# Optimization experiments

Measured on AMD Instinct MI355X. Metric: run time of the kernel, lower is better.

## Reference

```python
import jax, jax.numpy as jnp
import numpy as np

B, N, E, ED, H, HID, OUT = 128, 100, 3200, 8, 4, 16, 32


def _ln(x, g, b):
    m = x.mean(-1, keepdims=True)
    v = ((x - m) ** 2).mean(-1, keepdims=True)
    return (x - m) / jnp.sqrt(v + 1e-5) * g + b


def _seg_softmax(logits, seg, n):
    # logits: [Etot, H], seg: [Etot] target node ids
    m = jax.ops.segment_max(logits, seg, num_segments=n)
    ex = jnp.exp(logits - m[seg])
    s = jax.ops.segment_sum(ex, seg, num_segments=n)
    return ex / (s[seg] + 1e-16)


def _tconv(x, src, dst, ea, Wq, bq, Wk, bk, Wv, bv, We, Ws, bs, heads, ch, n):
    # PyG TransformerConv, concat=False, root_weight=True, beta=False
    q = (x @ Wq.T + bq).reshape(-1, heads, ch)
    k = (x @ Wk.T + bk).reshape(-1, heads, ch)
    v = (x @ Wv.T + bv).reshape(-1, heads, ch)
    e = (ea @ We.T).reshape(-1, heads, ch)
    alpha = (q[dst] * (k[src] + e)).sum(-1) / jnp.sqrt(jnp.float32(ch))  # [Etot,H]
    alpha = _seg_softmax(alpha, dst, n)
    msg = (v[src] + e) * alpha[..., None]
    out = jax.ops.segment_sum(msg, dst, num_segments=n)  # [n,H,ch]
    out = out.mean(axis=1)  # concat=False -> head mean
    return out + x @ Ws.T + bs


def setup_inputs() -> dict:
    key = jax.random.key(0)
    ks = jax.random.split(key, 32)
    d = {}
    d['nodes_feats'] = jax.random.randint(ks[0], (B, N, 1), 0, 5).astype(jnp.float32)
    d['edge_index'] = jax.random.randint(ks[1], (B, 2, E), 0, N).astype(jnp.int32)
    d['edge_attr'] = jax.random.normal(ks[2], (B, E, ED), jnp.float32)
    d['agent_id'] = jax.random.randint(ks[3], (B, 1), 0, N).astype(jnp.int32)
    s = 0.1
    d['entity_embed'] = jax.random.normal(ks[4], (5, 4), jnp.float32)
    d['W1'] = jax.random.normal(ks[5], (HID, 4 + ED), jnp.float32) * s
    d['b1'] = jnp.zeros((HID,), jnp.float32)
    d['W2'] = jax.random.normal(ks[6], (HID, HID), jnp.float32) * s
    d['b2'] = jnp.zeros((HID,), jnp.float32)
    d['W3'] = jax.random.normal(ks[7], (HID, HID), jnp.float32) * s
    d['b3'] = jnp.zeros((HID,), jnp.float32)
    d['ln_g'] = jnp.ones((HID,), jnp.float32)
    d['ln_b'] = jnp.zeros((HID,), jnp.float32)
    i = 8
    for pre, ch, outd in (('g1', HID, HID), ('g2', OUT, OUT)):
        d[pre + '_Wq'] = jax.random.normal(ks[i + 0], (H * ch, HID), jnp.float32) * s
        d[pre + '_bq'] = jnp.zeros((H * ch,), jnp.float32)
        d[pre + '_Wk'] = jax.random.normal(ks[i + 1], (H * ch, HID), jnp.float32) * s
        d[pre + '_bk'] = jnp.zeros((H * ch,), jnp.float32)
        d[pre + '_Wv'] = jax.random.normal(ks[i + 2], (H * ch, HID), jnp.float32) * s
        d[pre + '_bv'] = jnp.zeros((H * ch,), jnp.float32)
        d[pre + '_We'] = jax.random.normal(ks[i + 3], (H * ch, ED), jnp.float32) * s
        d[pre + '_Ws'] = jax.random.normal(ks[i + 4], (outd, HID), jnp.float32) * s
        d[pre + '_bs'] = jnp.zeros((outd,), jnp.float32)
        i += 5
    return d


def reference(nodes_feats, edge_index, edge_attr, agent_id, entity_embed,
              W1, b1, W2, b2, W3, b3, ln_g, ln_b,
              g1_Wq, g1_bq, g1_Wk, g1_bk, g1_Wv, g1_bv, g1_We, g1_Ws, g1_bs,
              g2_Wq, g2_bq, g2_Wk, g2_bk, g2_Wv, g2_bv, g2_We, g2_Ws, g2_bs):
    n_tot = B * N
    # batched graph -> flat graph with per-batch node offsets
    offs = (jnp.arange(B, dtype=edge_index.dtype) * N)[:, None, None]
    ei = (edge_index + offs).transpose(1, 0, 2).reshape(2, -1)  # [2, B*E]
    src, dst = ei[0], ei[1]
    x = nodes_feats.reshape(-1, 1)            # [n_tot, 1]
    ea = edge_attr.reshape(-1, ED)            # [B*E, ED]

    # Embedding message-passing layer (aggr='add')
    etype = x[:, 0].astype(jnp.int32)[src]
    emb = entity_embed[etype]                  # [Etot, 4]
    h = jnp.concatenate([emb, ea], axis=1)
    h = _ln(jax.nn.relu(h @ W1.T + b1), ln_g, ln_b)
    h = _ln(jax.nn.relu(h @ W2.T + b2), ln_g, ln_b)
    h = _ln(jax.nn.relu(h @ W3.T + b3), ln_g, ln_b)
    z = jax.ops.segment_sum(h, dst, num_segments=n_tot)  # [n_tot, 16]

    a = _tconv(z, src, dst, ea, g1_Wq, g1_bq, g1_Wk, g1_bk, g1_Wv, g1_bv,
               g1_We, g1_Ws, g1_bs, H, HID, n_tot)
    a = _tconv(a, src, dst, ea, g2_Wq, g2_bq, g2_Wk, g2_bk, g2_Wv, g2_bv,
               g2_We, g2_Ws, g2_bs, H, OUT, n_tot)
    a = jax.nn.relu(a).reshape(B, N, OUT)
    # graph_aggr == 'agent': gather the agent node per batch
    out = jnp.take_along_axis(a, agent_id[:, :, None].astype(jnp.int32), axis=1)
    return out[:, 0, :]  # [B, OUT]
```

## Files before the change

kernel.cpp:

```cpp
#include <hip/hip_runtime.h>
#include <math.h>
#include <stdint.h>

#define Bb   128
#define Nn   100
#define Ee   3200
#define NTOT (Bb*Nn)
#define ETOT (Bb*Ee)



__global__ __launch_bounds__(1024) void k_csr(const int* __restrict__ ei,
                                              const int* __restrict__ agent,
                                              int* __restrict__ off,
                                              int2* __restrict__ cpair,
                                              int* __restrict__ mark)
{
    int b = ((blockIdx.x & 7) << 4) + (blockIdx.x >> 3);
    int t = threadIdx.x;
    __shared__ int s_src[Ee];
    __shared__ int s_dst[Ee];
    __shared__ int cnt[128];
    __shared__ int exc[128];
    __shared__ int cur[128];
    if (t < 128) cnt[t] = 0;
    if (t < Nn) mark[b * Nn + t] = 0;
    __syncthreads();
    const int* eis = ei + (size_t)b * 2 * Ee;
    const int* eid = eis + Ee;
    for (int e = t; e < Ee; e += 1024) {
        int s = eis[e];
        int d = eid[e];
        s_src[e] = s;
        s_dst[e] = d;
        atomicAdd(&cnt[d], 1);
    }
    __syncthreads();
    if (t < 64) {
        int c0 = cnt[2 * t];
        int c1 = cnt[2 * t + 1];
        int p = c0 + c1;
#pragma unroll
        for (int d = 1; d < 64; d <<= 1) {
            int v = __shfl_up(p, d);
            if (t >= d) p += v;
        }
        exc[2 * t]     = p - c0 - c1;
        exc[2 * t + 1] = p - c1;
        cur[2 * t]     = p - c0 - c1;
        cur[2 * t + 1] = p - c1;
    }
    __syncthreads();
    if (t < Nn) off[b * Nn + t] = b * Ee + exc[t];
    if (b == Bb - 1 && t == 0) off[NTOT] = ETOT;
    for (int e = t; e < Ee; e += 1024) {
        int d = s_dst[e];
        int idx = atomicAdd(&cur[d], 1);
        cpair[b * Ee + idx] = make_int2(s_src[e] + b * Nn, b * Ee + e);
    }
    int an = agent[b];
    if (t == 0) mark[b * Nn + an] = 1;
    for (int e = t; e < Ee; e += 1024) {
        if (s_dst[e] == an) mark[b * Nn + s_src[e]] = 1;
    }
}


__device__ __forceinline__ void ln_reg(float* h, const float* __restrict__ g,
                                       const float* __restrict__ b) {
    float s = 0.f;
#pragma unroll
    for (int c = 0; c < 16; c++) s += h[c];
    float m = s * 0.0625f;
    float v = 0.f;
#pragma unroll
    for (int c = 0; c < 16; c++) { float d = h[c] - m; v += d * d; }
    float r = rsqrtf(v * 0.0625f + 1e-5f);
#pragma unroll
    for (int c = 0; c < 16; c++) h[c] = (h[c] - m) * r * g[c] + b[c];
}

__global__ __launch_bounds__(256) void k_mlpz(
    const float* __restrict__ nf, const float* __restrict__ ea, const float* __restrict__ ee,
    const float* __restrict__ W1, const float* __restrict__ b1,
    const float* __restrict__ W2, const float* __restrict__ b2,
    const float* __restrict__ W3, const float* __restrict__ b3,
    const float* __restrict__ lg, const float* __restrict__ lb,
    const float* __restrict__ Wk, const float* __restrict__ bk,
    const float* __restrict__ Wv, const float* __restrict__ bv,
    const int* __restrict__ off, const int2* __restrict__ cpair,
    float* __restrict__ z, float* __restrict__ k1, float* __restrict__ v1)
{
    int lane = threadIdx.x & 63;
    int wid  = threadIdx.x >> 6;
    int n    = (blockIdx.x & 7) * (NTOT / 8) + (blockIdx.x >> 3) * 4 + wid;

    int o0 = off[n];
    int deg = off[n + 1] - o0;
    int chunks = (deg + 63) >> 6;

    float zs[16];
#pragma unroll
    for (int c = 0; c < 16; c++) zs[c] = 0.f;

    for (int ch = 0; ch < chunks; ch++) {
        int i = ch * 64 + lane;
        float h3[16];
        if (i < deg) {
            int2 p = cpair[o0 + i];
            int et = (int)nf[p.x];
            float in[12];
#pragma unroll
            for (int j = 0; j < 4; j++) in[j] = ee[et * 4 + j];
            const float4* ea4 = (const float4*)(ea + (size_t)p.y * 8);
            float4 ua = ea4[0], ub = ea4[1];
            in[4] = ua.x; in[5] = ua.y; in[6] = ua.z; in[7] = ua.w;
            in[8] = ub.x; in[9] = ub.y; in[10] = ub.z; in[11] = ub.w;

            float h1[16];
#pragma unroll
            for (int c = 0; c < 16; c++) {
                float s = b1[c];
#pragma unroll
                for (int j = 0; j < 12; j++) s = fmaf(W1[c * 12 + j], in[j], s);
                h1[c] = fmaxf(s, 0.f);
            }
            ln_reg(h1, lg, lb);
            float h2[16];
#pragma unroll
            for (int c = 0; c < 16; c++) {
                float s = b2[c];
#pragma unroll
                for (int j = 0; j < 16; j++) s = fmaf(W2[c * 16 + j], h1[j], s);
                h2[c] = fmaxf(s, 0.f);
            }
            ln_reg(h2, lg, lb);
#pragma unroll
            for (int c = 0; c < 16; c++) {
                float s = b3[c];
#pragma unroll
                for (int j = 0; j < 16; j++) s = fmaf(W3[c * 16 + j], h2[j], s);
                h3[c] = fmaxf(s, 0.f);
            }
            ln_reg(h3, lg, lb);
        } else {
#pragma unroll
            for (int c = 0; c < 16; c++) h3[c] = 0.f;
        }
#pragma unroll
        for (int c = 0; c < 16; c++) {
            float s = h3[c];
            s += __shfl_xor(s, 1);
            s += __shfl_xor(s, 2);
            s += __shfl_xor(s, 4);
            s += __shfl_xor(s, 8);
            s += __shfl_xor(s, 16);
            s += __shfl_xor(s, 32);
            zs[c] += s;
        }
    }

#pragma unroll
    for (int c = 0; c < 16; c++) if (lane == c) z[n * 16 + c] = zs[c];

    float ak = bk[lane], av = bv[lane];
#pragma unroll
    for (int j = 0; j < 16; j++) {
        ak = fmaf(Wk[lane * 16 + j], zs[j], ak);
        av = fmaf(Wv[lane * 16 + j], zs[j], av);
    }
    k1[n * 64 + lane] = ak;
    v1[n * 64 + lane] = av;
}


__global__ __launch_bounds__(256) void k_attn1(
    const float* __restrict__ ea,
    const float* __restrict__ k1, const float* __restrict__ v1,
    const float* __restrict__ z, const int* __restrict__ mark,
    const float* __restrict__ Wq, const float* __restrict__ bq,
    const float* __restrict__ We, const float* __restrict__ Ws, const float* __restrict__ bs,
    const int* __restrict__ off, const int2* __restrict__ cpair,
    float* __restrict__ a1)
{
    int n = (blockIdx.x & 7) * (NTOT / 8) + (blockIdx.x >> 3);
    if (!mark[n]) return;

    __shared__ float sm[4][64], sl[4][64], sa[4][64];
    int lane = threadIdx.x & 63;
    int w    = threadIdx.x >> 6;

    float zz[16];
#pragma unroll
    for (int j = 0; j < 16; j++) zz[j] = z[n * 16 + j];
    float ql = bq[lane];
#pragma unroll
    for (int j = 0; j < 16; j++) ql = fmaf(Wq[lane * 16 + j], zz[j], ql);
    float wer[8];
#pragma unroll
    for (int j = 0; j < 8; j++) wer[j] = We[lane * 8 + j];

    int o0  = off[n];
    int deg = off[n + 1] - o0;
    int i    = o0 + ((deg * w) >> 2);
    int iend = o0 + ((deg * (w + 1)) >> 2);

    float m = -1e30f, l = 0.f, acc = 0.f;
    for (; i + 2 <= iend; i += 2) {
        int2 pA = cpair[i];
        int2 pB = cpair[i + 1];
        const float4* eaA = (const float4*)(ea + (size_t)pA.y * 8);
        const float4* eaB = (const float4*)(ea + (size_t)pB.y * 8);
        float4 a0v = eaA[0], a1v = eaA[1], b0v = eaB[0], b1v = eaB[1];
        float eA = wer[0] * a0v.x + wer[1] * a0v.y + wer[2] * a0v.z + wer[3] * a0v.w
                 + wer[4] * a1v.x + wer[5] * a1v.y + wer[6] * a1v.z + wer[7] * a1v.w;
        float eB = wer[0] * b0v.x + wer[1] * b0v.y + wer[2] * b0v.z + wer[3] * b0v.w
                 + wer[4] * b1v.x + wer[5] * b1v.y + wer[6] * b1v.z + wer[7] * b1v.w;
        float kA = k1[(size_t)pA.x * 64 + lane];
        float kB = k1[(size_t)pB.x * 64 + lane];
        float vA = v1[(size_t)pA.x * 64 + lane];
        float vB = v1[(size_t)pB.x * 64 + lane];
        float tA = ql * (kA + eA);
        float tB = ql * (kB + eB);
        tA += __shfl_xor(tA, 1, 16);  tB += __shfl_xor(tB, 1, 16);
        tA += __shfl_xor(tA, 2, 16);  tB += __shfl_xor(tB, 2, 16);
        tA += __shfl_xor(tA, 4, 16);  tB += __shfl_xor(tB, 4, 16);
        tA += __shfl_xor(tA, 8, 16);  tB += __shfl_xor(tB, 8, 16);
        float lA  = tA * 0.25f;
        float lBv = tB * 0.25f;
        float nm = fmaxf(m, fmaxf(lA, lBv));
        float sc = __expf(m - nm);
        float wA = __expf(lA - nm);
        float wB = __expf(lBv - nm);
        acc = acc * sc + wA * (vA + eA) + wB * (vB + eB);
        l   = l * sc + wA + wB;
        m   = nm;
    }
    for (; i < iend; i++) {
        int2 p = cpair[i];
        const float4* ea4 = (const float4*)(ea + (size_t)p.y * 8);
        float4 u0 = ea4[0], u1 = ea4[1];
        float el = wer[0] * u0.x + wer[1] * u0.y + wer[2] * u0.z + wer[3] * u0.w
                 + wer[4] * u1.x + wer[5] * u1.y + wer[6] * u1.z + wer[7] * u1.w;
        float kl = k1[(size_t)p.x * 64 + lane];
        float tq = ql * (kl + el);
        tq += __shfl_xor(tq, 1, 16);
        tq += __shfl_xor(tq, 2, 16);
        tq += __shfl_xor(tq, 4, 16);
        tq += __shfl_xor(tq, 8, 16);
        float logit = tq * 0.25f;
        float nm = fmaxf(m, logit);
        float sc = __expf(m - nm);
        float wv = __expf(logit - nm);
        float vl = v1[(size_t)p.x * 64 + lane];
        acc = acc * sc + wv * (vl + el);
        l   = l * sc + wv;
        m   = nm;
    }
    sm[w][lane] = m; sl[w][lane] = l; sa[w][lane] = acc;
    __syncthreads();
    if (w == 0) {
        float M = fmaxf(fmaxf(sm[0][lane], sm[1][lane]), fmaxf(sm[2][lane], sm[3][lane]));
        float L = 0.f, A = 0.f;
#pragma unroll
        for (int ww = 0; ww < 4; ww++) {
            float sc = __expf(sm[ww][lane] - M);
            L += sc * sl[ww][lane];
            A += sc * sa[ww][lane];
        }
        float y = (deg > 0) ? (A / L) : 0.f;
        y += __shfl_xor(y, 16);
        y += __shfl_xor(y, 32);
        y *= 0.25f;
        if (lane < 16) {
            float r = bs[lane];
#pragma unroll
            for (int j = 0; j < 16; j++) r = fmaf(Ws[lane * 16 + j], zz[j], r);
            a1[n * 16 + lane] = y + r;
        }
    }
}


__global__ __launch_bounds__(512) void k_g2(
    const float* __restrict__ ea, const float* __restrict__ a1, const int* __restrict__ agent,
    const float* __restrict__ Wq, const float* __restrict__ bq,
    const float* __restrict__ Wk, const float* __restrict__ bk,
    const float* __restrict__ Wv, const float* __restrict__ bv,
    const float* __restrict__ We, const float* __restrict__ Ws, const float* __restrict__ bs,
    const int* __restrict__ off, const int2* __restrict__ cpair,
    float* __restrict__ out)
{
    __shared__ float sm[8][64], sl[8][64], sa0[8][64], sa1[8][64];
    int b = ((blockIdx.x & 7) << 4) + (blockIdx.x >> 3);
    int lane = threadIdx.x & 63;
    int w = threadIdx.x >> 6;
    int n = b * Nn + agent[b];
    int v0 = lane * 2, v1i = lane * 2 + 1;

    float aa[16];
#pragma unroll
    for (int j = 0; j < 16; j++) aa[j] = a1[n * 16 + j];

    float wk0[16], wk1[16], wv0[16], wv1[16], we0[8], we1[8];
#pragma unroll
    for (int j = 0; j < 16; j++) {
        wk0[j] = Wk[v0 * 16 + j];  wk1[j] = Wk[v1i * 16 + j];
        wv0[j] = Wv[v0 * 16 + j];  wv1[j] = Wv[v1i * 16 + j];
    }
#pragma unroll
    for (int j = 0; j < 8; j++) { we0[j] = We[v0 * 8 + j]; we1[j] = We[v1i * 8 + j]; }

    float q0 = bq[v0], q1v = bq[v1i];
#pragma unroll
    for (int j = 0; j < 16; j++) {
        q0  = fmaf(Wq[v0 * 16 + j],  aa[j], q0);
        q1v = fmaf(Wq[v1i * 16 + j], aa[j], q1v);
    }

    int o0 = off[n];
    int deg = off[n + 1] - o0;

    float m = -1e30f, l = 0.f, a0 = 0.f, a1c = 0.f;
    for (int i = w; i < deg; i += 8) {
        int2 p = cpair[o0 + i];
        int src = p.x, ge = p.y;
        float as[16];
#pragma unroll
        for (int j = 0; j < 16; j++) as[j] = a1[src * 16 + j];
        const float4* ea4 = (const float4*)(ea + (size_t)ge * 8);
        float4 u0 = ea4[0], u1 = ea4[1];
        float eav[8] = {u0.x, u0.y, u0.z, u0.w, u1.x, u1.y, u1.z, u1.w};

        float k0 = bk[v0], k1v = bk[v1i], vv0 = bv[v0], vv1 = bv[v1i];
#pragma unroll
        for (int j = 0; j < 16; j++) {
            k0  = fmaf(wk0[j], as[j], k0);
            k1v = fmaf(wk1[j], as[j], k1v);
            vv0 = fmaf(wv0[j], as[j], vv0);
            vv1 = fmaf(wv1[j], as[j], vv1);
        }
        float e0 = 0.f, e1 = 0.f;
#pragma unroll
        for (int j = 0; j < 8; j++) { e0 = fmaf(we0[j], eav[j], e0); e1 = fmaf(we1[j], eav[j], e1); }

        float t = q0 * (k0 + e0) + q1v * (k1v + e1);
        t += __shfl_xor(t, 1, 16);
        t += __shfl_xor(t, 2, 16);
        t += __shfl_xor(t, 4, 16);
        t += __shfl_xor(t, 8, 16);
        float logit = t * 0.17677669529663687f;
        float nm = fmaxf(m, logit);
        float sc = __expf(m - nm);
        float wgt = __expf(logit - nm);
        a0  = a0 * sc + wgt * (vv0 + e0);
        a1c = a1c * sc + wgt * (vv1 + e1);
        l   = l * sc + wgt;
        m   = nm;
    }
    sm[w][lane] = m; sl[w][lane] = l; sa0[w][lane] = a0; sa1[w][lane] = a1c;
    __syncthreads();
    if (w == 0) {
        float M = sm[0][lane];
#pragma unroll
        for (int ww = 1; ww < 8; ww++) M = fmaxf(M, sm[ww][lane]);
        float L = 0.f, A0 = 0.f, A1 = 0.f;
#pragma unroll
        for (int ww = 0; ww < 8; ww++) {
            float sc = __expf(sm[ww][lane] - M);
            L  += sc * sl[ww][lane];
            A0 += sc * sa0[ww][lane];
            A1 += sc * sa1[ww][lane];
        }
        float y0 = (deg > 0) ? (A0 / L) : 0.f;
        float y1 = (deg > 0) ? (A1 / L) : 0.f;
        y0 += __shfl_xor(y0, 16); y0 += __shfl_xor(y0, 32);
        y1 += __shfl_xor(y1, 16); y1 += __shfl_xor(y1, 32);
        y0 *= 0.25f; y1 *= 0.25f;

        if (lane < 16) {
            int c0 = lane * 2, c1 = lane * 2 + 1;
            float r0 = bs[c0], r1 = bs[c1];
#pragma unroll
            for (int j = 0; j < 16; j++) {
                r0 = fmaf(Ws[c0 * 16 + j], aa[j], r0);
                r1 = fmaf(Ws[c1 * 16 + j], aa[j], r1);
            }
            out[b * 32 + c0] = fmaxf(y0 + r0, 0.f);
            out[b * 32 + c1] = fmaxf(y1 + r1, 0.f);
        }
    }
}


extern "C" void kernel_launch(void* const* d_in, const int* in_sizes, int n_in,
                              void* d_out, int out_size, void* d_ws, size_t ws_size,
                              hipStream_t stream) {
    (void)in_sizes; (void)n_in; (void)out_size; (void)ws_size;
    const float* nf    = (const float*)d_in[0];
    const int*   ei    = (const int*)d_in[1];
    const float* ea    = (const float*)d_in[2];
    const int*   agent = (const int*)d_in[3];
    const float* ee    = (const float*)d_in[4];
    const float* W1    = (const float*)d_in[5];
    const float* b1    = (const float*)d_in[6];
    const float* W2    = (const float*)d_in[7];
    const float* b2    = (const float*)d_in[8];
    const float* W3    = (const float*)d_in[9];
    const float* b3    = (const float*)d_in[10];
    const float* lg    = (const float*)d_in[11];
    const float* lb    = (const float*)d_in[12];
    const float* g1Wq  = (const float*)d_in[13];
    const float* g1bq  = (const float*)d_in[14];
    const float* g1Wk  = (const float*)d_in[15];
    const float* g1bk  = (const float*)d_in[16];
    const float* g1Wv  = (const float*)d_in[17];
    const float* g1bv  = (const float*)d_in[18];
    const float* g1We  = (const float*)d_in[19];
    const float* g1Ws  = (const float*)d_in[20];
    const float* g1bs  = (const float*)d_in[21];
    const float* g2Wq  = (const float*)d_in[22];
    const float* g2bq  = (const float*)d_in[23];
    const float* g2Wk  = (const float*)d_in[24];
    const float* g2bk  = (const float*)d_in[25];
    const float* g2Wv  = (const float*)d_in[26];
    const float* g2bv  = (const float*)d_in[27];
    const float* g2We  = (const float*)d_in[28];
    const float* g2Ws  = (const float*)d_in[29];
    const float* g2bs  = (const float*)d_in[30];
    float* out = (float*)d_out;

    char* w = (char*)d_ws;
    int* mark  = (int*)w;  w += (size_t)NTOT * 4;
    int* off   = (int*)w;  w += (size_t)(NTOT + 4) * 4;
    w = (char*)(((uintptr_t)w + 15) & ~(uintptr_t)15);
    int2* cpair = (int2*)w; w += (size_t)ETOT * 8;
    float* z   = (float*)w; w += (size_t)NTOT * 16 * 4;
    float* k1  = (float*)w; w += (size_t)NTOT * 64 * 4;
    float* v1  = (float*)w; w += (size_t)NTOT * 64 * 4;
    float* a1  = (float*)w; w += (size_t)NTOT * 16 * 4;

    k_csr<<<dim3(Bb), dim3(1024), 0, stream>>>(ei, agent, off, cpair, mark);
    k_mlpz<<<dim3(NTOT / 4), dim3(256), 0, stream>>>(
        nf, ea, ee, W1, b1, W2, b2, W3, b3, lg, lb,
        g1Wk, g1bk, g1Wv, g1bv,
        off, cpair, z, k1, v1);
    k_attn1<<<dim3(NTOT), dim3(256), 0, stream>>>(
        ea, k1, v1, z, mark,
        g1Wq, g1bq, g1We, g1Ws, g1bs,
        off, cpair, a1);
    k_g2<<<dim3(Bb), dim3(512), 0, stream>>>(
        ea, a1, agent, g2Wq, g2bq, g2Wk, g2bk, g2Wv, g2bv, g2We, g2Ws, g2bs,
        off, cpair, out);
}
```

Before: 193.7 us.

## Fuse CSR build with edge MLP and compact marked-node list for attention

Merges the CSR construction kernel and the per-node edge-MLP/z aggregation into one kernel per graph. That kernel computes the edge MLP in original edge order, reduces z with shared-memory atomics, and computes k1/v1 from shared z. It also builds a compact list of nodes that need layer-1 attention, so attn1 launches 128*50 blocks that loop over listed nodes instead of NTOT blocks that mostly exit early. This removes one launch and the CSR gather indirection in the MLP. In exchange, 128 blocks of 512 threads may underfill the GPU for the MLP work, and shared atomics can contend.

```diff
diff --git a/kernel.cpp b/kernel.cpp
--- a/kernel.cpp
+++ b/kernel.cpp
@@ -9,63 +9,6 @@
 #define ETOT (Bb*Ee)
 
 
-
-__global__ __launch_bounds__(1024) void k_csr(const int* __restrict__ ei,
-                                              const int* __restrict__ agent,
-                                              int* __restrict__ off,
-                                              int2* __restrict__ cpair,
-                                              int* __restrict__ mark)
-{
-    int b = ((blockIdx.x & 7) << 4) + (blockIdx.x >> 3);
-    int t = threadIdx.x;
-    __shared__ int s_src[Ee];
-    __shared__ int s_dst[Ee];
-    __shared__ int cnt[128];
-    __shared__ int exc[128];
-    __shared__ int cur[128];
-    if (t < 128) cnt[t] = 0;
-    if (t < Nn) mark[b * Nn + t] = 0;
-    __syncthreads();
-    const int* eis = ei + (size_t)b * 2 * Ee;
-    const int* eid = eis + Ee;
-    for (int e = t; e < Ee; e += 1024) {
-        int s = eis[e];
-        int d = eid[e];
-        s_src[e] = s;
-        s_dst[e] = d;
-        atomicAdd(&cnt[d], 1);
-    }
-    __syncthreads();
-    if (t < 64) {
-        int c0 = cnt[2 * t];
-        int c1 = cnt[2 * t + 1];
-        int p = c0 + c1;
-#pragma unroll
-        for (int d = 1; d < 64; d <<= 1) {
-            int v = __shfl_up(p, d);
-            if (t >= d) p += v;
-        }
-        exc[2 * t]     = p - c0 - c1;
-        exc[2 * t + 1] = p - c1;
-        cur[2 * t]     = p - c0 - c1;
-        cur[2 * t + 1] = p - c1;
-    }
-    __syncthreads();
-    if (t < Nn) off[b * Nn + t] = b * Ee + exc[t];
-    if (b == Bb - 1 && t == 0) off[NTOT] = ETOT;
-    for (int e = t; e < Ee; e += 1024) {
-        int d = s_dst[e];
-        int idx = atomicAdd(&cur[d], 1);
-        cpair[b * Ee + idx] = make_int2(s_src[e] + b * Nn, b * Ee + e);
-    }
-    int an = agent[b];
-    if (t == 0) mark[b * Nn + an] = 1;
-    for (int e = t; e < Ee; e += 1024) {
-        if (s_dst[e] == an) mark[b * Nn + s_src[e]] = 1;
-    }
-}
-
-
 __device__ __forceinline__ void ln_reg(float* h, const float* __restrict__ g,
                                        const float* __restrict__ b) {
     float s = 0.f;
@@ -80,7 +23,9 @@
     for (int c = 0; c < 16; c++) h[c] = (h[c] - m) * r * g[c] + b[c];
 }
 
-__global__ __launch_bounds__(256) void k_mlpz(
+
+__global__ __launch_bounds__(512) void k_cmz(
+    const int* __restrict__ ei, const int* __restrict__ agent,
     const float* __restrict__ nf, const float* __restrict__ ea, const float* __restrict__ ee,
     const float* __restrict__ W1, const float* __restrict__ b1,
     const float* __restrict__ W2, const float* __restrict__ b2,
@@ -88,196 +33,256 @@
     const float* __restrict__ lg, const float* __restrict__ lb,
     const float* __restrict__ Wk, const float* __restrict__ bk,
     const float* __restrict__ Wv, const float* __restrict__ bv,
-    const int* __restrict__ off, const int2* __restrict__ cpair,
+    int* __restrict__ off, int2* __restrict__ cpair,
+    int* __restrict__ mlist, int* __restrict__ mcnt,
     float* __restrict__ z, float* __restrict__ k1, float* __restrict__ v1)
 {
-    int lane = threadIdx.x & 63;
-    int wid  = threadIdx.x >> 6;
-    int n    = (blockIdx.x & 7) * (NTOT / 8) + (blockIdx.x >> 3) * 4 + wid;
-
-    int o0 = off[n];
-    int deg = off[n + 1] - o0;
-    int chunks = (deg + 63) >> 6;
-
-    float zs[16];
-#pragma unroll
-    for (int c = 0; c < 16; c++) zs[c] = 0.f;
-
-    for (int ch = 0; ch < chunks; ch++) {
-        int i = ch * 64 + lane;
+    int b = ((blockIdx.x & 7) << 4) + (blockIdx.x >> 3);
+    int t = threadIdx.x;
+    __shared__ int   s_src[Ee];
+    __shared__ int   s_dst[Ee];
+    __shared__ float zl[Nn][17];
+    __shared__ int   cnt[128], exc[128], cur[128];
+    __shared__ int   smark[Nn], slist[Nn];
+    __shared__ int   scnt;
+
+    for (int i = t; i < Nn * 17; i += 512) ((float*)zl)[i] = 0.f;
+    if (t < 128) cnt[t] = 0;
+    if (t < Nn)  smark[t] = 0;
+    if (t == 0)  scnt = 0;
+    __syncthreads();
+
+    const int* eis = ei + (size_t)b * 2 * Ee;
+    const int* eid = eis + Ee;
+    for (int e = t; e < Ee; e += 512) {
+        int s = eis[e];
+        int d = eid[e];
+        s_src[e] = s;
+        s_dst[e] = d;
+        atomicAdd(&cnt[d], 1);
+    }
+    __syncthreads();
+    if (t < 64) {
+        int c0 = cnt[2 * t];
+        int c1 = cnt[2 * t + 1];
+        int p = c0 + c1;
+#pragma unroll
+        for (int d = 1; d < 64; d <<= 1) {
+            int v = __shfl_up(p, d);
+            if (t >= d) p += v;
+        }
+        exc[2 * t]     = p - c0 - c1;
+        exc[2 * t + 1] = p - c1;
+        cur[2 * t]     = p - c0 - c1;
+        cur[2 * t + 1] = p - c1;
+    }
+    __syncthreads();
+    if (t < Nn) off[b * Nn + t] = b * Ee + exc[t];
+    if (b == Bb - 1 && t == 0) off[NTOT] = ETOT;
+    for (int e = t; e < Ee; e += 512) {
+        int d = s_dst[e];
+        int idx = atomicAdd(&cur[d], 1);
+        cpair[b * Ee + idx] = make_int2(s_src[e] + b * Nn, b * Ee + e);
+    }
+    int an = agent[b];
+    if (t == 0) {
+        int old = atomicExch(&smark[an], 1);
+        if (!old) { int ix = atomicAdd(&scnt, 1); slist[ix] = an; }
+    }
+    for (int e = t; e < Ee; e += 512) {
+        if (s_dst[e] == an) {
+            int s = s_src[e];
+            int old = atomicExch(&smark[s], 1);
+            if (!old) { int ix = atomicAdd(&scnt, 1); slist[ix] = s; }
+        }
+    }
+    for (int e = t; e < Ee; e += 512) {
+        int src = s_src[e];
+        int dst = s_dst[e];
+        int et = (int)nf[b * Nn + src];
+        float in[12];
+#pragma unroll
+        for (int j = 0; j < 4; j++) in[j] = ee[et * 4 + j];
+        const float4* ea4 = (const float4*)(ea + ((size_t)b * Ee + e) * 8);
+        float4 ua = ea4[0], ub = ea4[1];
+        in[4] = ua.x; in[5] = ua.y; in[6] = ua.z; in[7] = ua.w;
+        in[8] = ub.x; in[9] = ub.y; in[10] = ub.z; in[11] = ub.w;
+
+        float h1[16];
+#pragma unroll
+        for (int c = 0; c < 16; c++) {
+            float s = b1[c];
+#pragma unroll
+            for (int j = 0; j < 12; j++) s = fmaf(W1[c * 12 + j], in[j], s);
+            h1[c] = fmaxf(s, 0.f);
+        }
+        ln_reg(h1, lg, lb);
+        float h2[16];
+#pragma unroll
+        for (int c = 0; c < 16; c++) {
+            float s = b2[c];
+#pragma unroll
+            for (int j = 0; j < 16; j++) s = fmaf(W2[c * 16 + j], h1[j], s);
+            h2[c] = fmaxf(s, 0.f);
+        }
+        ln_reg(h2, lg, lb);
         float h3[16];
-        if (i < deg) {
-            int2 p = cpair[o0 + i];
-            int et = (int)nf[p.x];
-            float in[12];
-#pragma unroll
-            for (int j = 0; j < 4; j++) in[j] = ee[et * 4 + j];
-            const float4* ea4 = (const float4*)(ea + (size_t)p.y * 8);
-            float4 ua = ea4[0], ub = ea4[1];
-            in[4] = ua.x; in[5] = ua.y; in[6] = ua.z; in[7] = ua.w;
-            in[8] = ub.x; in[9] = ub.y; in[10] = ub.z; in[11] = ub.w;
-
-            float h1[16];
-#pragma unroll
-            for (int c = 0; c < 16; c++) {
-                float s = b1[c];
-#pragma unroll
-                for (int j = 0; j < 12; j++) s = fmaf(W1[c * 12 + j], in[j], s);
-                h1[c] = fmaxf(s, 0.f);
+#pragma unroll
+        for (int c = 0; c < 16; c++) {
+            float s = b3[c];
+#pragma unroll
+            for (int j = 0; j < 16; j++) s = fmaf(W3[c * 16 + j], h2[j], s);
+            h3[c] = fmaxf(s, 0.f);
+        }
+        ln_reg(h3, lg, lb);
+#pragma unroll
+        for (int c = 0; c < 16; c++) atomicAdd(&zl[dst][c], h3[c]);
+    }
+    __syncthreads();
+
+    if (t < scnt) mlist[b * Nn + t] = slist[t];
+    if (t == 0)   mcnt[b] = scnt;
+
+    {
+        int ch = t & 63;
+        int n0 = t >> 6;
+        float wkr[16], wvr[16];
+#pragma unroll
+        for (int j = 0; j < 16; j++) { wkr[j] = Wk[ch * 16 + j]; wvr[j] = Wv[ch * 16 + j]; }
+        float bkv = bk[ch], bvv = bv[ch];
+        for (int n = n0; n < Nn; n += 8) {
+            float zz[16];
+#pragma unroll
+            for (int j = 0; j < 16; j++) zz[j] = zl[n][j];
+            if (ch < 16) z[((size_t)b * Nn + n) * 16 + ch] = zl[n][ch];
+            float ak = bkv, av = bvv;
+#pragma unroll
+            for (int j = 0; j < 16; j++) {
+                ak = fmaf(wkr[j], zz[j], ak);
+                av = fmaf(wvr[j], zz[j], av);
             }
-            ln_reg(h1, lg, lb);
-            float h2[16];
-#pragma unroll
-            for (int c = 0; c < 16; c++) {
-                float s = b2[c];
-#pragma unroll
-                for (int j = 0; j < 16; j++) s = fmaf(W2[c * 16 + j], h1[j], s);
-                h2[c] = fmaxf(s, 0.f);
-            }
-            ln_reg(h2, lg, lb);
-#pragma unroll
-            for (int c = 0; c < 16; c++) {
-                float s = b3[c];
-#pragma unroll
-                for (int j = 0; j < 16; j++) s = fmaf(W3[c * 16 + j], h2[j], s);
-                h3[c] = fmaxf(s, 0.f);
-            }
-            ln_reg(h3, lg, lb);
-        } else {
-#pragma unroll
-            for (int c = 0; c < 16; c++) h3[c] = 0.f;
-        }
-#pragma unroll
-        for (int c = 0; c < 16; c++) {
-            float s = h3[c];
-            s += __shfl_xor(s, 1);
-            s += __shfl_xor(s, 2);
-            s += __shfl_xor(s, 4);
-            s += __shfl_xor(s, 8);
-            s += __shfl_xor(s, 16);
-            s += __shfl_xor(s, 32);
-            zs[c] += s;
-        }
-    }
-
-#pragma unroll
-    for (int c = 0; c < 16; c++) if (lane == c) z[n * 16 + c] = zs[c];
-
-    float ak = bk[lane], av = bv[lane];
-#pragma unroll
-    for (int j = 0; j < 16; j++) {
-        ak = fmaf(Wk[lane * 16 + j], zs[j], ak);
-        av = fmaf(Wv[lane * 16 + j], zs[j], av);
-    }
-    k1[n * 64 + lane] = ak;
-    v1[n * 64 + lane] = av;
+            k1[((size_t)b * Nn + n) * 64 + ch] = ak;
+            v1[((size_t)b * Nn + n) * 64 + ch] = av;
+        }
+    }
 }
 
 
 __global__ __launch_bounds__(256) void k_attn1(
     const float* __restrict__ ea,
     const float* __restrict__ k1, const float* __restrict__ v1,
-    const float* __restrict__ z, const int* __restrict__ mark,
+    const float* __restrict__ z,
+    const int* __restrict__ mlist, const int* __restrict__ mcnt,
     const float* __restrict__ Wq, const float* __restrict__ bq,
     const float* __restrict__ We, const float* __restrict__ Ws, const float* __restrict__ bs,
     const int* __restrict__ off, const int2* __restrict__ cpair,
     float* __restrict__ a1)
 {
-    int n = (blockIdx.x & 7) * (NTOT / 8) + (blockIdx.x >> 3);
-    if (!mark[n]) return;
-
     __shared__ float sm[4][64], sl[4][64], sa[4][64];
+    int bl   = blockIdx.x & 127;
+    int rep  = blockIdx.x >> 7;
+    int b    = ((bl & 7) << 4) + (bl >> 3);
     int lane = threadIdx.x & 63;
     int w    = threadIdx.x >> 6;
-
-    float zz[16];
-#pragma unroll
-    for (int j = 0; j < 16; j++) zz[j] = z[n * 16 + j];
-    float ql = bq[lane];
-#pragma unroll
-    for (int j = 0; j < 16; j++) ql = fmaf(Wq[lane * 16 + j], zz[j], ql);
-    float wer[8];
+    int mc   = mcnt[b];
+
+    float wq[16], wer[8];
+#pragma unroll
+    for (int j = 0; j < 16; j++) wq[j] = Wq[lane * 16 + j];
 #pragma unroll
     for (int j = 0; j < 8; j++) wer[j] = We[lane * 8 + j];
-
-    int o0  = off[n];
-    int deg = off[n + 1] - o0;
-    int i    = o0 + ((deg * w) >> 2);
-    int iend = o0 + ((deg * (w + 1)) >> 2);
-
-    float m = -1e30f, l = 0.f, acc = 0.f;
-    for (; i + 2 <= iend; i += 2) {
-        int2 pA = cpair[i];
-        int2 pB = cpair[i + 1];
-        const float4* eaA = (const float4*)(ea + (size_t)pA.y * 8);
-        const float4* eaB = (const float4*)(ea + (size_t)pB.y * 8);
-        float4 a0v = eaA[0], a1v = eaA[1], b0v = eaB[0], b1v = eaB[1];
-        float eA = wer[0] * a0v.x + wer[1] * a0v.y + wer[2] * a0v.z + wer[3] * a0v.w
-                 + wer[4] * a1v.x + wer[5] * a1v.y + wer[6] * a1v.z + wer[7] * a1v.w;
-        float eB = wer[0] * b0v.x + wer[1] * b0v.y + wer[2] * b0v.z + wer[3] * b0v.w
-                 + wer[4] * b1v.x + wer[5] * b1v.y + wer[6] * b1v.z + wer[7] * b1v.w;
-        float kA = k1[(size_t)pA.x * 64 + lane];
-        float kB = k1[(size_t)pB.x * 64 + lane];
-        float vA = v1[(size_t)pA.x * 64 + lane];
-        float vB = v1[(size_t)pB.x * 64 + lane];
-        float tA = ql * (kA + eA);
-        float tB = ql * (kB + eB);
-        tA += __shfl_xor(tA, 1, 16);  tB += __shfl_xor(tB, 1, 16);
-        tA += __shfl_xor(tA, 2, 16);  tB += __shfl_xor(tB, 2, 16);
-        tA += __shfl_xor(tA, 4, 16);  tB += __shfl_xor(tB, 4, 16);
-        tA += __shfl_xor(tA, 8, 16);  tB += __shfl_xor(tB, 8, 16);
-        float lA  = tA * 0.25f;
-        float lBv = tB * 0.25f;
-        float nm = fmaxf(m, fmaxf(lA, lBv));
-        float sc = __expf(m - nm);
-        float wA = __expf(lA - nm);
-        float wB = __expf(lBv - nm);
-        acc = acc * sc + wA * (vA + eA) + wB * (vB + eB);
-        l   = l * sc + wA + wB;
-        m   = nm;
-    }
-    for (; i < iend; i++) {
-        int2 p = cpair[i];
-        const float4* ea4 = (const float4*)(ea + (size_t)p.y * 8);
-        float4 u0 = ea4[0], u1 = ea4[1];
-        float el = wer[0] * u0.x + wer[1] * u0.y + wer[2] * u0.z + wer[3] * u0.w
-                 + wer[4] * u1.x + wer[5] * u1.y + wer[6] * u1.z + wer[7] * u1.w;
-        float kl = k1[(size_t)p.x * 64 + lane];
-        float tq = ql * (kl + el);
-        tq += __shfl_xor(tq, 1, 16);
-        tq += __shfl_xor(tq, 2, 16);
-        tq += __shfl_xor(tq, 4, 16);
-        tq += __shfl_xor(tq, 8, 16);
-        float logit = tq * 0.25f;
-        float nm = fmaxf(m, logit);
-        float sc = __expf(m - nm);
-        float wv = __expf(logit - nm);
-        float vl = v1[(size_t)p.x * 64 + lane];
-        acc = acc * sc + wv * (vl + el);
-        l   = l * sc + wv;
-        m   = nm;
-    }
-    sm[w][lane] = m; sl[w][lane] = l; sa[w][lane] = acc;
-    __syncthreads();
-    if (w == 0) {
-        float M = fmaxf(fmaxf(sm[0][lane], sm[1][lane]), fmaxf(sm[2][lane], sm[3][lane]));
-        float L = 0.f, A = 0.f;
-#pragma unroll
-        for (int ww = 0; ww < 4; ww++) {
-            float sc = __expf(sm[ww][lane] - M);
-            L += sc * sl[ww][lane];
-            A += sc * sa[ww][lane];
-        }
-        float y = (deg > 0) ? (A / L) : 0.f;
-        y += __shfl_xor(y, 16);
-        y += __shfl_xor(y, 32);
-        y *= 0.25f;
-        if (lane < 16) {
-            float r = bs[lane];
-#pragma unroll
-            for (int j = 0; j < 16; j++) r = fmaf(Ws[lane * 16 + j], zz[j], r);
-            a1[n * 16 + lane] = y + r;
-        }
+    float bq1 = bq[lane];
+
+    for (int ix = rep; ix < mc; ix += 50) {
+        int n = b * Nn + mlist[b * Nn + ix];
+
+        float zz[16];
+#pragma unroll
+        for (int j = 0; j < 16; j++) zz[j] = z[n * 16 + j];
+        float ql = bq1;
+#pragma unroll
+        for (int j = 0; j < 16; j++) ql = fmaf(wq[j], zz[j], ql);
+
+        int o0  = off[n];
+        int deg = off[n + 1] - o0;
+        int i    = o0 + ((deg * w) >> 2);
+        int iend = o0 + ((deg * (w + 1)) >> 2);
+
+        float m = -1e30f, l = 0.f, acc = 0.f;
+        for (; i + 2 <= iend; i += 2) {
+            int2 pA = cpair[i];
+            int2 pB = cpair[i + 1];
+            const float4* eaA = (const float4*)(ea + (size_t)pA.y * 8);
+            const float4* eaB = (const float4*)(ea + (size_t)pB.y * 8);
+            float4 a0v = eaA[0], a1v = eaA[1], b0v = eaB[0], b1v = eaB[1];
+            float eA = wer[0] * a0v.x + wer[1] * a0v.y + wer[2] * a0v.z + wer[3] * a0v.w
+                     + wer[4] * a1v.x + wer[5] * a1v.y + wer[6] * a1v.z + wer[7] * a1v.w;
+            float eB = wer[0] * b0v.x + wer[1] * b0v.y + wer[2] * b0v.z + wer[3] * b0v.w
+                     + wer[4] * b1v.x + wer[5] * b1v.y + wer[6] * b1v.z + wer[7] * b1v.w;
+            float kA = k1[(size_t)pA.x * 64 + lane];
+            float kB = k1[(size_t)pB.x * 64 + lane];
+            float vA = v1[(size_t)pA.x * 64 + lane];
+            float vB = v1[(size_t)pB.x * 64 + lane];
+            float tA = ql * (kA + eA);
+            float tB = ql * (kB + eB);
+            tA += __shfl_xor(tA, 1, 16);  tB += __shfl_xor(tB, 1, 16);
+            tA += __shfl_xor(tA, 2, 16);  tB += __shfl_xor(tB, 2, 16);
+            tA += __shfl_xor(tA, 4, 16);  tB += __shfl_xor(tB, 4, 16);
+            tA += __shfl_xor(tA, 8, 16);  tB += __shfl_xor(tB, 8, 16);
+            float lA  = tA * 0.25f;
+            float lBv = tB * 0.25f;
+            float nm = fmaxf(m, fmaxf(lA, lBv));
+            float sc = __expf(m - nm);
+            float wA = __expf(lA - nm);
+            float wB = __expf(lBv - nm);
+            acc = acc * sc + wA * (vA + eA) + wB * (vB + eB);
+            l   = l * sc + wA + wB;
+            m   = nm;
+        }
+        for (; i < iend; i++) {
+            int2 p = cpair[i];
+            const float4* ea4 = (const float4*)(ea + (size_t)p.y * 8);
+            float4 u0 = ea4[0], u1 = ea4[1];
+            float el = wer[0] * u0.x + wer[1] * u0.y + wer[2] * u0.z + wer[3] * u0.w
+                     + wer[4] * u1.x + wer[5] * u1.y + wer[6] * u1.z + wer[7] * u1.w;
+            float kl = k1[(size_t)p.x * 64 + lane];
+            float tq = ql * (kl + el);
+            tq += __shfl_xor(tq, 1, 16);
+            tq += __shfl_xor(tq, 2, 16);
+            tq += __shfl_xor(tq, 4, 16);
+            tq += __shfl_xor(tq, 8, 16);
+            float logit = tq * 0.25f;
+            float nm = fmaxf(m, logit);
+            float sc = __expf(m - nm);
+            float wv = __expf(logit - nm);
+            float vl = v1[(size_t)p.x * 64 + lane];
+            acc = acc * sc + wv * (vl + el);
+            l   = l * sc + wv;
+            m   = nm;
+        }
+        sm[w][lane] = m; sl[w][lane] = l; sa[w][lane] = acc;
+        __syncthreads();
+        if (w == 0) {
+            float M = fmaxf(fmaxf(sm[0][lane], sm[1][lane]), fmaxf(sm[2][lane], sm[3][lane]));
+            float L = 0.f, A = 0.f;
+#pragma unroll
+            for (int ww = 0; ww < 4; ww++) {
+                float sc = __expf(sm[ww][lane] - M);
+                L += sc * sl[ww][lane];
+                A += sc * sa[ww][lane];
+            }
+            float y = (deg > 0) ? (A / L) : 0.f;
+            y += __shfl_xor(y, 16);
+            y += __shfl_xor(y, 32);
+            y *= 0.25f;
+            if (lane < 16) {
+                float r = bs[lane];
+#pragma unroll
+                for (int j = 0; j < 16; j++) r = fmaf(Ws[lane * 16 + j], zz[j], r);
+                a1[n * 16 + lane] = y + r;
+            }
+        }
+        __syncthreads();
     }
 }
 
@@ -324,11 +329,10 @@
     float m = -1e30f, l = 0.f, a0 = 0.f, a1c = 0.f;
     for (int i = w; i < deg; i += 8) {
         int2 p = cpair[o0 + i];
-        int src = p.x, ge = p.y;
         float as[16];
 #pragma unroll
-        for (int j = 0; j < 16; j++) as[j] = a1[src * 16 + j];
-        const float4* ea4 = (const float4*)(ea + (size_t)ge * 8);
+        for (int j = 0; j < 16; j++) as[j] = a1[(size_t)p.x * 16 + j];
+        const float4* ea4 = (const float4*)(ea + (size_t)p.y * 8);
         float4 u0 = ea4[0], u1 = ea4[1];
         float eav[8] = {u0.x, u0.y, u0.z, u0.w, u1.x, u1.y, u1.z, u1.w};
 
@@ -431,7 +435,6 @@
     float* out = (float*)d_out;
 
     char* w = (char*)d_ws;
-    int* mark  = (int*)w;  w += (size_t)NTOT * 4;
     int* off   = (int*)w;  w += (size_t)(NTOT + 4) * 4;
     w = (char*)(((uintptr_t)w + 15) & ~(uintptr_t)15);
     int2* cpair = (int2*)w; w += (size_t)ETOT * 8;
@@ -439,14 +442,16 @@
     float* k1  = (float*)w; w += (size_t)NTOT * 64 * 4;
     float* v1  = (float*)w; w += (size_t)NTOT * 64 * 4;
     float* a1  = (float*)w; w += (size_t)NTOT * 16 * 4;
-
-    k_csr<<<dim3(Bb), dim3(1024), 0, stream>>>(ei, agent, off, cpair, mark);
-    k_mlpz<<<dim3(NTOT / 4), dim3(256), 0, stream>>>(
-        nf, ea, ee, W1, b1, W2, b2, W3, b3, lg, lb,
+    int* mlist = (int*)w;  w += (size_t)NTOT * 4;
+    int* mcnt  = (int*)w;  w += (size_t)Bb * 4;
+
+    k_cmz<<<dim3(Bb), dim3(512), 0, stream>>>(
+        ei, agent, nf, ea, ee,
+        W1, b1, W2, b2, W3, b3, lg, lb,
         g1Wk, g1bk, g1Wv, g1bv,
-        off, cpair, z, k1, v1);
-    k_attn1<<<dim3(NTOT), dim3(256), 0, stream>>>(
-        ea, k1, v1, z, mark,
+        off, cpair, mlist, mcnt, z, k1, v1);
+    k_attn1<<<dim3(Bb * 50), dim3(256), 0, stream>>>(
+        ea, k1, v1, z, mlist, mcnt,
         g1Wq, g1bq, g1We, g1Ws, g1bs,
         off, cpair, a1);
     k_g2<<<dim3(Bb), dim3(512), 0, stream>>>(
```

Measured after the change: 397.5 us. 105% more time.
